# Performance work log

Hardware: AMD Instinct MI355X
Metric: run time of the kernel (lower is better)

Reference implementation:

```python
import jax, jax.numpy as jnp
import numpy as np

D_MODEL = 1024
NUM_EXPERTS = 8


def setup_inputs() -> dict:
    key = jax.random.key(0)
    k_x, k_wg, k_bg, k_we, k_be = jax.random.split(key, 5)
    B, S, D, E = 4, 2048, D_MODEL, NUM_EXPERTS
    x = jax.random.normal(k_x, (B, S, D), dtype=jnp.float32)
    # gate: nn.Linear(d_model, num_experts) -> weight [E, D], bias [E]
    Wg = jax.random.normal(k_wg, (E, D), dtype=jnp.float32) * 0.02
    bg = jax.random.normal(k_bg, (E,), dtype=jnp.float32) * 0.02
    # experts: E x nn.Linear(d_model, d_model) -> weights [E, D, D], biases [E, D]
    We = jax.random.normal(k_we, (E, D, D), dtype=jnp.float32) * 0.02
    be = jax.random.normal(k_be, (E, D), dtype=jnp.float32) * 0.02
    return {"x": x, "Wg": Wg, "bg": bg, "We": We, "be": be, "top_k": 2}


def reference(x, Wg, bg, We, be, top_k):
    # gate_scores: softmax over experts. x:[B,S,D], Wg:[E,D] -> [B,S,E]
    gate_scores = jax.nn.softmax(jnp.einsum("bsd,ed->bse", x, Wg) + bg, axis=-1)
    top_k_values, top_k_indices = jax.lax.top_k(gate_scores, top_k)  # [B,S,K]
    # dense all-expert compute (faithful to original): [B,S,D,E]
    expert_outputs = jnp.einsum("bsd,ekd->bske", x, We) + be.T  # be.T: [D,E]
    # gather top-k experts along last dim: idx broadcast over feature dim D
    top_k_outputs = jnp.take_along_axis(
        expert_outputs, top_k_indices[:, :, None, :], axis=-1
    )  # [B,S,D,K]
    weighted = (top_k_outputs * top_k_values[:, :, None, :]).sum(axis=-1)  # [B,S,D]
    return weighted
```

## Files before the change

### kernel.cpp

```cpp
#include <hip/hip_runtime.h>
#include <hip/hip_bf16.h>
#include <stdint.h>

#define D_MODEL 1024
#define NUM_EXPERTS 8
#define NBUCKET 16
#define BM 128
#define BN 128
#define BK 64
#define GATE_TOK 16

typedef __bf16 bf16x8 __attribute__((ext_vector_type(8)));
typedef float f32x4 __attribute__((ext_vector_type(4)));

__device__ __forceinline__ unsigned short f32_to_bf16_rne(float f) {
    union { float f; uint32_t u; } v;
    v.f = f;
    uint32_t u = v.u;
    u += 0x7FFFu + ((u >> 16) & 1u);
    return (unsigned short)(u >> 16);
}

__device__ __forceinline__ float bf16_to_f32(unsigned short h) {
    union { uint32_t u; float f; } v;
    v.u = ((uint32_t)h) << 16;
    return v.f;
}

__device__ __forceinline__ void gload_lds16(const unsigned short* g, unsigned short* l) {
    __builtin_amdgcn_global_load_lds(
        (const __attribute__((address_space(1))) void*)g,
        (__attribute__((address_space(3))) void*)l,
        16, 0, 0);
}

__global__ __launch_bounds__(256) void prep_kernel(
    const float* __restrict__ x, const float* __restrict__ Wg,
    const float* __restrict__ bg, const float* __restrict__ We,
    unsigned short* __restrict__ wbv, int T,
    int* __restrict__ counts, int* __restrict__ token_list,
    float* __restrict__ gate_list, unsigned short* __restrict__ xb,
    int nconv)
{
    const int tid = threadIdx.x;

    if ((int)blockIdx.x < nconv) {
        int i = blockIdx.x * 256 + tid;
        float4 f = ((const float4*)We)[i];
        ushort4 o;
        o.x = f32_to_bf16_rne(f.x);
        o.y = f32_to_bf16_rne(f.y);
        o.z = f32_to_bf16_rne(f.z);
        o.w = f32_to_bf16_rne(f.w);
        ((ushort4*)wbv)[i] = o;
        return;
    }

    const int gb   = blockIdx.x - nconv;
    const int lane = tid & 63;
    const int wave = tid >> 6;
    const int tokBase = gb * GATE_TOK;

    __shared__ float4 WgS[NUM_EXPERTS * 256];
    __shared__ double logitS[GATE_TOK][NUM_EXPERTS];
    __shared__ int cntS[NBUCKET];
    __shared__ int baseS[NBUCKET];

    if (tid < NBUCKET) cntS[tid] = 0;
#pragma unroll
    for (int i = 0; i < 8; i++)
        WgS[i * 256 + tid] = ((const float4*)Wg)[i * 256 + tid];
    __syncthreads();

    for (int tt = 0; tt < GATE_TOK / 4; tt++) {
        const int lt = wave * (GATE_TOK / 4) + tt;
        const int token = tokBase + lt;
        const float4* xr4 = (const float4*)(x + (size_t)token * D_MODEL);
        ushort4* xbr4 = (ushort4*)(xb + (size_t)token * D_MODEL);

        float4 xv[4];
#pragma unroll
        for (int q = 0; q < 4; q++) {
            float4 f = xr4[q * 64 + lane];
            xv[q] = f;
            ushort4 o;
            o.x = f32_to_bf16_rne(f.x);
            o.y = f32_to_bf16_rne(f.y);
            o.z = f32_to_bf16_rne(f.z);
            o.w = f32_to_bf16_rne(f.w);
            xbr4[q * 64 + lane] = o;
        }

        double acc[NUM_EXPERTS];
#pragma unroll
        for (int e = 0; e < NUM_EXPERTS; e++) {
            double a = 0.0;
#pragma unroll
            for (int q = 0; q < 4; q++) {
                float4 w = WgS[e * 256 + q * 64 + lane];
                a += (double)xv[q].x * (double)w.x;
                a += (double)xv[q].y * (double)w.y;
                a += (double)xv[q].z * (double)w.z;
                a += (double)xv[q].w * (double)w.w;
            }
            acc[e] = a;
        }
#pragma unroll
        for (int e = 0; e < NUM_EXPERTS; e++) {
            double a = acc[e];
            for (int off = 32; off > 0; off >>= 1) a += __shfl_xor(a, off, 64);
            acc[e] = a;
        }
        if (lane == 0) {
#pragma unroll
            for (int e = 0; e < NUM_EXPERTS; e++)
                logitS[lt][e] = acc[e] + (double)bg[e];
        }
    }
    __syncthreads();

    int i1 = 0, i2 = 0, o1 = 0, o2 = 0;
    double v1d = 0.0, v2d = 0.0;
    const int token2 = tokBase + tid;
    if (tid < GATE_TOK) {
        double lg[NUM_EXPERTS];
#pragma unroll
        for (int e = 0; e < NUM_EXPERTS; e++) lg[e] = logitS[tid][e];
        i1 = 0;
#pragma unroll
        for (int e = 1; e < NUM_EXPERTS; e++) if (lg[e] > lg[i1]) i1 = e;
        i2 = (i1 == 0) ? 1 : 0;
#pragma unroll
        for (int e = 0; e < NUM_EXPERTS; e++)
            if (e != i1 && lg[e] > lg[i2]) i2 = e;
        double m = lg[i1], den = 0.0;
#pragma unroll
        for (int e = 0; e < NUM_EXPERTS; e++) den += exp(lg[e] - m);
        v1d = exp(lg[i1] - m) / den;
        v2d = exp(lg[i2] - m) / den;
        o1 = atomicAdd(&cntS[i1], 1);
        o2 = atomicAdd(&cntS[8 + i2], 1);
    }
    __syncthreads();
    if (tid < NBUCKET) baseS[tid] = atomicAdd(&counts[tid], cntS[tid]);
    __syncthreads();
    if (tid < GATE_TOK) {
        int p1 = i1 * T + baseS[i1] + o1;
        token_list[p1] = token2;
        gate_list[p1]  = (float)v1d;
        int p2 = (8 + i2) * T + baseS[8 + i2] + o2;
        token_list[p2] = token2;
        gate_list[p2]  = (float)v2d;
    }
}

__global__ __launch_bounds__(256) void moe_gemm(
    const unsigned short* __restrict__ xb,
    const unsigned short* __restrict__ wb,
    const float* __restrict__ be,
    const int* __restrict__ counts,
    const int* __restrict__ token_list,
    const float* __restrict__ gate_list,
    unsigned short* __restrict__ ybuf,
    int T)
{
    const int bid = blockIdx.x;
    const int vexp = bid & 15;
    const int mt = (bid >> 4) & 63;
    const int nt = bid >> 10;
    const int e_w = vexp & 7;

    const int n_e = counts[vexp];
    const int m0 = mt * BM;
    if (m0 >= n_e) return;
    const int n0 = nt * BN;
    const int tid = threadIdx.x;

    __shared__ __align__(16) unsigned short As[BM * BK];
    __shared__ __align__(16) unsigned short Bs[BN * BK];

    const unsigned short* asrc[4];
    const unsigned short* bsrc[4];
    const unsigned short* wbase = wb + (size_t)e_w * D_MODEL * D_MODEL;
    const int* tl = token_list + vexp * T;
    const float* gl = gate_list + vexp * T;
#pragma unroll
    for (int i = 0; i < 4; i++) {
        int flat = i * 256 + tid;
        int r = flat >> 3, seg = flat & 7;
        int ss = seg ^ (r & 7);
        int gr = m0 + r;
        int tk = (gr < n_e) ? tl[gr] : 0;
        asrc[i] = xb + (size_t)tk * D_MODEL + ss * 8;
        bsrc[i] = wbase + (size_t)(n0 + r) * D_MODEL + ss * 8;
    }

    const int wave = tid >> 6, lane = tid & 63;
    const int wm = (wave >> 1) * 64, wn = (wave & 1) * 64;
    const int frow = lane & 15;
    const int qq = lane >> 4;
    const int sw8 = frow & 7;
    const int col = lane & 15;

    float bev[4];
#pragma unroll
    for (int ni = 0; ni < 4; ni++)
        bev[ni] = be[e_w * D_MODEL + n0 + wn + ni * 16 + col];

    f32x4 acc[4][4];
#pragma unroll
    for (int mi = 0; mi < 4; mi++)
#pragma unroll
        for (int ni = 0; ni < 4; ni++)
            acc[mi][ni] = (f32x4){0.f, 0.f, 0.f, 0.f};

    for (int kt = 0; kt < D_MODEL / BK; kt++) {
        const int k0 = kt * BK;
#pragma unroll
        for (int i = 0; i < 4; i++) {
            int flat = i * 256 + tid;
            gload_lds16(asrc[i] + k0, &As[flat * 8]);
            gload_lds16(bsrc[i] + k0, &Bs[flat * 8]);
        }
        __syncthreads();
#pragma unroll
        for (int ks = 0; ks < 2; ks++) {
            const int off = ((ks * 4 + qq) ^ sw8) * 8;
            bf16x8 af[4], bfv[4];
#pragma unroll
            for (int mi = 0; mi < 4; mi++)
                af[mi] = *(const bf16x8*)&As[(wm + mi * 16 + frow) * BK + off];
#pragma unroll
            for (int ni = 0; ni < 4; ni++)
                bfv[ni] = *(const bf16x8*)&Bs[(wn + ni * 16 + frow) * BK + off];
#pragma unroll
            for (int mi = 0; mi < 4; mi++)
#pragma unroll
                for (int ni = 0; ni < 4; ni++)
                    acc[mi][ni] = __builtin_amdgcn_mfma_f32_16x16x32_bf16(
                        af[mi], bfv[ni], acc[mi][ni], 0, 0, 0);
        }
        __syncthreads();
    }

    unsigned short* ybase = ybuf + (size_t)(vexp >> 3) * T * D_MODEL;
    const int rbase = (lane >> 4) * 4;
#pragma unroll
    for (int mi = 0; mi < 4; mi++) {
#pragma unroll
        for (int r = 0; r < 4; r++) {
            int lrow = wm + mi * 16 + rbase + r;
            int gr = m0 + lrow;
            if (gr < n_e) {
                int   tk = tl[gr];
                float gv = gl[gr];
                unsigned short* yr = ybase + (size_t)tk * D_MODEL;
#pragma unroll
                for (int ni = 0; ni < 4; ni++) {
                    int c = n0 + wn + ni * 16 + col;
                    yr[c] = f32_to_bf16_rne(gv * (acc[mi][ni][r] + bev[ni]));
                }
            }
        }
    }
}

__global__ __launch_bounds__(256) void combine_kernel(
    const unsigned short* __restrict__ y0,
    const unsigned short* __restrict__ y1,
    float* __restrict__ out, int n4)
{
    int i = blockIdx.x * 256 + threadIdx.x;
    if (i >= n4) return;
    ushort4 a = ((const ushort4*)y0)[i];
    ushort4 b = ((const ushort4*)y1)[i];
    float4 o;
    o.x = bf16_to_f32(a.x) + bf16_to_f32(b.x);
    o.y = bf16_to_f32(a.y) + bf16_to_f32(b.y);
    o.z = bf16_to_f32(a.z) + bf16_to_f32(b.z);
    o.w = bf16_to_f32(a.w) + bf16_to_f32(b.w);
    ((float4*)out)[i] = o;
}

extern "C" void kernel_launch(void* const* d_in, const int* in_sizes, int n_in,
                              void* d_out, int out_size, void* d_ws, size_t ws_size,
                              hipStream_t stream) {
    const float* x  = (const float*)d_in[0];
    const float* Wg = (const float*)d_in[1];
    const float* bg = (const float*)d_in[2];
    const float* We = (const float*)d_in[3];
    const float* be = (const float*)d_in[4];

    const int T = in_sizes[0] / D_MODEL;

    char* ws = (char*)d_ws;
    unsigned short* xb = (unsigned short*)ws;
    size_t off = (size_t)T * D_MODEL * 2;
    unsigned short* wbv = (unsigned short*)(ws + off);
    off += (size_t)NUM_EXPERTS * D_MODEL * D_MODEL * 2;
    int* counts = (int*)(ws + off);         off += 256;
    int* token_list = (int*)(ws + off);     off += (size_t)NBUCKET * T * 4;
    float* gate_list = (float*)(ws + off);  off += (size_t)NBUCKET * T * 4;
    unsigned short* ybuf = (unsigned short*)(ws + off);
    off += (size_t)2 * T * D_MODEL * 2;

    hipMemsetAsync(counts, 0, 256, stream);

    const int nconv = NUM_EXPERTS * D_MODEL * D_MODEL / 4 / 256;
    const int ngate = T / GATE_TOK;
    prep_kernel<<<nconv + ngate, 256, 0, stream>>>(
        x, Wg, bg, We, wbv, T, counts, token_list, gate_list, xb, nconv);

    moe_gemm<<<8 * 64 * 16, 256, 0, stream>>>(
        xb, wbv, be, counts, token_list, gate_list, ybuf, T);

    int n4c = T * D_MODEL / 4;
    combine_kernel<<<(n4c + 255) / 256, 256, 0, stream>>>(
        ybuf, ybuf + (size_t)T * D_MODEL, (float*)d_out, n4c);
}
```

Baseline: 228.9 us.

## Register-prefetch GEMM tiles, reorder block index, use float softmax

The MoE GEMM drops direct global-to-LDS loads for register staging. The next K tile is loaded into registers while MFMAs run on the current tile in LDS, so global latency overlaps compute. Block index decoding now puts the N tile innermost, so neighbouring blocks share the same gathered token rows. The gate softmax uses float __expf instead of double exp. The trade-off is more registers per thread and less precise gate weights.

Measured after the change: 350.8 us. 1.53x slower.

```diff
diff --git a/kernel.cpp b/kernel.cpp
--- a/kernel.cpp
+++ b/kernel.cpp
@@ -25,13 +25,6 @@
     union { uint32_t u; float f; } v;
     v.u = ((uint32_t)h) << 16;
     return v.f;
-}
-
-__device__ __forceinline__ void gload_lds16(const unsigned short* g, unsigned short* l) {
-    __builtin_amdgcn_global_load_lds(
-        (const __attribute__((address_space(1))) void*)g,
-        (__attribute__((address_space(3))) void*)l,
-        16, 0, 0);
 }
 
 __global__ __launch_bounds__(256) void prep_kernel(
@@ -120,7 +113,7 @@
     __syncthreads();
 
     int i1 = 0, i2 = 0, o1 = 0, o2 = 0;
-    double v1d = 0.0, v2d = 0.0;
+    float v1 = 0.f, v2 = 0.f;
     const int token2 = tokBase + tid;
     if (tid < GATE_TOK) {
         double lg[NUM_EXPERTS];
@@ -133,11 +126,12 @@
 #pragma unroll
         for (int e = 0; e < NUM_EXPERTS; e++)
             if (e != i1 && lg[e] > lg[i2]) i2 = e;
-        double m = lg[i1], den = 0.0;
-#pragma unroll
-        for (int e = 0; e < NUM_EXPERTS; e++) den += exp(lg[e] - m);
-        v1d = exp(lg[i1] - m) / den;
-        v2d = exp(lg[i2] - m) / den;
+        double m = lg[i1];
+        float den = 0.f;
+#pragma unroll
+        for (int e = 0; e < NUM_EXPERTS; e++) den += __expf((float)(lg[e] - m));
+        v1 = __expf((float)(lg[i1] - m)) / den;
+        v2 = __expf((float)(lg[i2] - m)) / den;
         o1 = atomicAdd(&cntS[i1], 1);
         o2 = atomicAdd(&cntS[8 + i2], 1);
     }
@@ -147,10 +141,10 @@
     if (tid < GATE_TOK) {
         int p1 = i1 * T + baseS[i1] + o1;
         token_list[p1] = token2;
-        gate_list[p1]  = (float)v1d;
+        gate_list[p1]  = v1;
         int p2 = (8 + i2) * T + baseS[8 + i2] + o2;
         token_list[p2] = token2;
-        gate_list[p2]  = (float)v2d;
+        gate_list[p2]  = v2;
     }
 }
 
@@ -165,9 +159,10 @@
     int T)
 {
     const int bid = blockIdx.x;
-    const int vexp = bid & 15;
-    const int mt = (bid >> 4) & 63;
-    const int nt = bid >> 10;
+    const int nt = bid & 7;
+    const int rest = bid >> 3;
+    const int vexp = rest & 15;
+    const int mt = rest >> 4;
     const int e_w = vexp & 7;
 
     const int n_e = counts[vexp];
@@ -179,11 +174,10 @@
     __shared__ __align__(16) unsigned short As[BM * BK];
     __shared__ __align__(16) unsigned short Bs[BN * BK];
 
-    const unsigned short* asrc[4];
-    const unsigned short* bsrc[4];
     const unsigned short* wbase = wb + (size_t)e_w * D_MODEL * D_MODEL;
     const int* tl = token_list + vexp * T;
     const float* gl = gate_list + vexp * T;
+    uint32_t aoff[4], boff[4];
 #pragma unroll
     for (int i = 0; i < 4; i++) {
         int flat = i * 256 + tid;
@@ -191,8 +185,8 @@
         int ss = seg ^ (r & 7);
         int gr = m0 + r;
         int tk = (gr < n_e) ? tl[gr] : 0;
-        asrc[i] = xb + (size_t)tk * D_MODEL + ss * 8;
-        bsrc[i] = wbase + (size_t)(n0 + r) * D_MODEL + ss * 8;
+        aoff[i] = ((uint32_t)tk * D_MODEL + ss * 8) * 2;
+        boff[i] = (((uint32_t)(n0 + r)) * D_MODEL + ss * 8) * 2;
     }
 
     const int wave = tid >> 6, lane = tid & 63;
@@ -214,15 +208,31 @@
         for (int ni = 0; ni < 4; ni++)
             acc[mi][ni] = (f32x4){0.f, 0.f, 0.f, 0.f};
 
+    uint4 areg[4], breg[4];
+#pragma unroll
+    for (int i = 0; i < 4; i++) {
+        areg[i] = *(const uint4*)((const char*)xb    + aoff[i]);
+        breg[i] = *(const uint4*)((const char*)wbase + boff[i]);
+    }
+
     for (int kt = 0; kt < D_MODEL / BK; kt++) {
-        const int k0 = kt * BK;
+        __syncthreads();
 #pragma unroll
         for (int i = 0; i < 4; i++) {
-            int flat = i * 256 + tid;
-            gload_lds16(asrc[i] + k0, &As[flat * 8]);
-            gload_lds16(bsrc[i] + k0, &Bs[flat * 8]);
+            ((uint4*)As)[i * 256 + tid] = areg[i];
+            ((uint4*)Bs)[i * 256 + tid] = breg[i];
         }
         __syncthreads();
+
+        if (kt < D_MODEL / BK - 1) {
+            const uint32_t k1 = (uint32_t)(kt + 1) * BK * 2;
+#pragma unroll
+            for (int i = 0; i < 4; i++) {
+                areg[i] = *(const uint4*)((const char*)xb    + aoff[i] + k1);
+                breg[i] = *(const uint4*)((const char*)wbase + boff[i] + k1);
+            }
+        }
+
 #pragma unroll
         for (int ks = 0; ks < 2; ks++) {
             const int off = ((ks * 4 + qq) ^ sw8) * 8;
@@ -240,7 +250,6 @@
                     acc[mi][ni] = __builtin_amdgcn_mfma_f32_16x16x32_bf16(
                         af[mi], bfv[ni], acc[mi][ni], 0, 0, 0);
         }
-        __syncthreads();
     }
 
     unsigned short* ybase = ybuf + (size_t)(vexp >> 3) * T * D_MODEL;
@@ -311,7 +320,7 @@
     prep_kernel<<<nconv + ngate, 256, 0, stream>>>(
         x, Wg, bg, We, wbv, T, counts, token_list, gate_list, xb, nconv);
 
-    moe_gemm<<<8 * 64 * 16, 256, 0, stream>>>(
+    moe_gemm<<<8 * 16 * 64, 256, 0, stream>>>(
         xb, wbv, be, counts, token_list, gate_list, ybuf, T);
 
     int n4c = T * D_MODEL / 4;
```
